# Kernel tuning notes

Measured on AMD Instinct MI355X. Metric: run time of the kernel, lower is better.

## Reference

```python
import jax, jax.numpy as jnp
import numpy as np

PAD_TOKEN = 0.0
REPLACEMENT_PROB = 0.1


def setup_inputs() -> dict:
    key = jax.random.key(0)
    # item-ID-like values in [0, 100000); zeros act as pad tokens
    x = jax.random.randint(key, (16384, 2048), 0, 100000).astype(jnp.float32)
    return {"x": x}


def reference(x):
    """Stochastic Swap Noise: replace ~p of non-pad positions with values
    sampled without replacement from the non-pad values of the tensor.

    Jit-friendly equivalent of torch's
      bernoulli -> masked_select compaction -> randperm -> scatter
    chain: a single argsort on random keys (pads keyed to +2.0) both
    compacts the non-pad values to the front AND shuffles them; a cumsum
    over the replacement mask assigns each replaced position its donor.
    """
    key = jax.random.key(42)
    k_bern, k_shuf = jax.random.split(key)

    nonpad = x != PAD_TOKEN                                        # [B,S] bool
    repl = (jax.random.uniform(k_bern, x.shape) < REPLACEMENT_PROB) & nonpad

    flat_x = x.reshape(-1)                                          # [N]
    flat_nonpad = nonpad.reshape(-1)
    flat_repl = repl.reshape(-1)

    # compaction + shuffle in one sort: non-pad elems get uniform [0,1) keys,
    # pads get 2.0 so they sink to the end.
    r = jnp.where(flat_nonpad, jax.random.uniform(k_shuf, flat_x.shape), 2.0)
    order = jnp.argsort(r)
    donors = flat_x[order]                                          # shuffled non-pad values first

    # k-th replaced position (in flat order) takes donors[k]
    rank = jnp.cumsum(flat_repl) - 1                                # -1 where not replaced (masked out below)
    out = jnp.where(flat_repl, donors[rank], flat_x)
    return out.reshape(x.shape)
```

## Files before the change

### kernel.cpp

```cpp
#include <hip/hip_runtime.h>
#include <stdint.h>

static __host__ __device__ inline uint32_t rotl32(uint32_t x, int r) {
#if defined(__HIP_DEVICE_COMPILE__)
  return __builtin_amdgcn_alignbit(x, x, (uint32_t)(32 - r));
#else
  return (x << r) | (x >> (32 - r));
#endif
}

static __host__ __device__ inline void tf2x32(uint32_t k0, uint32_t k1,
                                              uint32_t x0, uint32_t x1,
                                              uint32_t& o0, uint32_t& o1) {
  uint32_t k2 = k0 ^ k1 ^ 0x1BD11BDAu;
#define TFR(a) { x0 += x1; x1 = rotl32(x1, a); x1 ^= x0; }
  x0 += k0; x1 += k1;
  TFR(13) TFR(15) TFR(26) TFR(6)
  x0 += k1; x1 += k2 + 1u;
  TFR(17) TFR(29) TFR(16) TFR(24)
  x0 += k2; x1 += k0 + 2u;
  TFR(13) TFR(15) TFR(26) TFR(6)
  x0 += k0; x1 += k1 + 3u;
  TFR(17) TFR(29) TFR(16) TFR(24)
  x0 += k1; x1 += k2 + 4u;
  TFR(13) TFR(15) TFR(26) TFR(6)
  x0 += k2; x1 += k0 + 5u;
#undef TFR
  o0 = x0; o1 = x1;
}

static __device__ inline uint32_t fold_bits(uint32_t k0, uint32_t k1, uint32_t ctr) {
  uint32_t a, b;
  tf2x32(k0, k1, 0u, ctr, a, b);
  return a ^ b;
}

#define CUT2      917504u
#define NBINS2    896u
#define NH        1024
#define ELEMS_G   8192
#define GPOOL     1216u
#define BSCAP     4608u
#define WIN       8192
#define CAPDUMP   3932160u
#define STRIDE    4608u
#define MASKI     0x07FFFFFFu
#define BERN_THR  838861u



template<bool BOUNDS>
__global__ __launch_bounds__(256, 6) void k_gen(const float* __restrict__ x,
                                                uint64_t* __restrict__ mask,
                                                uint32_t* __restrict__ rsums,
                                                uint32_t* __restrict__ dumpCursor,
                                                uint2* __restrict__ dump,
                                                uint32_t bk0, uint32_t bk1,
                                                uint32_t sk0, uint32_t sk1, int n) {
  __shared__ uint2 pool[GPOOL];
  __shared__ uint32_t wcnt[4];
  __shared__ uint32_t lpoolCnt, lgbase;
  int tid = threadIdx.x, lane = tid & 63, wid = tid >> 6;
  int base = blockIdx.x * ELEMS_G;
  if (tid == 0) lpoolCnt = 0;
  __syncthreads();

  uint32_t cnt = 0;
  unsigned long long bball[4];
  for (int it = 0; it < ELEMS_G / 1024; it++) {
    int e0 = base + it * 1024 + wid * 256 + lane * 4;
    float4 xv;
    if (!BOUNDS || e0 + 3 < n) {
      xv = *reinterpret_cast<const float4*>(x + e0);
    } else {
      xv.x = (e0 + 0 < n) ? x[e0 + 0] : 0.0f;
      xv.y = (e0 + 1 < n) ? x[e0 + 1] : 0.0f;
      xv.z = (e0 + 2 < n) ? x[e0 + 2] : 0.0f;
      xv.w = (e0 + 3 < n) ? x[e0 + 3] : 0.0f;
    }
#define GENE(e, comp)                                                     \
    {                                                                     \
      uint32_t ii = (uint32_t)(e0 + e);                                   \
      bool np = (comp != 0.0f);                                           \
      uint32_t bb = fold_bits(bk0, bk1, ii);                              \
      bool rr = np && ((bb >> 9) < BERN_THR);                             \
      bball[e] = __ballot(rr);                                            \
      uint32_t mm = fold_bits(sk0, sk1, ii) >> 9;                         \
      if (np && mm < CUT2) {                                              \
        uint32_t slot = atomicAdd(&lpoolCnt, 1u);                         \
        uint32_t v = (uint32_t)comp;                                      \
        if (slot < GPOOL)                                                 \
          pool[slot] = make_uint2((mm << 12) | (v >> 5),                  \
                                  ((v & 31u) << 27) | ii);                \
      }                                                                   \
    }
    GENE(0, xv.x) GENE(1, xv.y) GENE(2, xv.z) GENE(3, xv.w)
#undef GENE
    cnt += (uint32_t)(__popcll(bball[0]) + __popcll(bball[1]) +
                      __popcll(bball[2]) + __popcll(bball[3]));
    if (lane == 0) {
      uint32_t ci = (uint32_t)blockIdx.x * 32u + (uint32_t)it * 4u + (uint32_t)wid;
      if (!BOUNDS) {
        mask[ci * 4 + 0] = bball[0]; mask[ci * 4 + 1] = bball[1];
        mask[ci * 4 + 2] = bball[2]; mask[ci * 4 + 3] = bball[3];
      } else {
        for (int e = 0; e < 4; e++)
          if ((int)(ci * 256u + (uint32_t)e * 64u) < n) mask[ci * 4 + e] = bball[e];
      }
    }
  }
  if (lane == 0) wcnt[wid] = cnt;
  __syncthreads();
  if (tid == 0) {
    rsums[blockIdx.x] = wcnt[0] + wcnt[1] + wcnt[2] + wcnt[3];
    uint32_t pc = lpoolCnt; if (pc > GPOOL) pc = GPOOL;
    lgbase = atomicAdd((unsigned int*)dumpCursor, pc);
  }
  __syncthreads();
  uint32_t pc = lpoolCnt; if (pc > GPOOL) pc = GPOOL;
  uint32_t gb = lgbase;
  for (uint32_t j = tid; j < pc; j += 256) {
    uint32_t d = gb + j;
    if (d < CAPDUMP) dump[d] = pool[j];
  }
}

__global__ void k_scan2(uint32_t* __restrict__ data0, int n0,
                        uint32_t* __restrict__ data1, int n1) {
  __shared__ uint32_t wsum[4];
  uint32_t* data = (blockIdx.x == 0) ? data0 : data1;
  int n = (blockIdx.x == 0) ? n0 : n1;
  int tid = threadIdx.x, lane = tid & 63, wid = tid >> 6;
  uint32_t running = 0;
  for (int base = 0; base < n; base += 256) {
    int i = base + tid;
    uint32_t v = (i < n) ? data[i] : 0u;
    uint32_t incl = v;
    for (int d = 1; d < 64; d <<= 1) {
      uint32_t t = __shfl_up(incl, (unsigned)d, 64);
      if (lane >= d) incl += t;
    }
    if (lane == 63) wsum[wid] = incl;
    __syncthreads();
    uint32_t woff = 0, tot = 0;
    for (int w = 0; w < 4; w++) { uint32_t s = wsum[w]; if (w < wid) woff += s; tot += s; }
    if (i < n) data[i] = running + woff + (incl - v);
    running += tot;
    __syncthreads();
  }
  if (tid == 0) data[n] = running;
}

__global__ __launch_bounds__(256) void k_regroup(const uint2* __restrict__ dump,
                                                 const uint32_t* __restrict__ dumpCursor,
                                                 uint32_t* __restrict__ fineCursor,
                                                 uint2* __restrict__ fine) {
  __shared__ uint2    pool2[WIN];
  __shared__ uint32_t lhist[NH];
  __shared__ uint32_t lgbase[NH];
  __shared__ uint32_t wsums[4];
  int tid = threadIdx.x, lane = tid & 63, wid = tid >> 6;
  uint32_t total = dumpCursor[0];
  if (total > CAPDUMP) total = CAPDUMP;
  uint32_t wbase = blockIdx.x * (uint32_t)WIN;
  if (wbase >= total) return;
  uint32_t valid = total - wbase;
  if (valid > WIN) valid = WIN;

  for (int b = tid; b < NH; b += 256) lhist[b] = 0;
  __syncthreads();
  uint2 e[WIN / 256];
#pragma unroll
  for (int q = 0; q < WIN / 256; q++) {
    uint32_t j = (uint32_t)q * 256u + (uint32_t)tid;
    e[q] = (j < valid) ? dump[wbase + j] : make_uint2(0u, 0u);
    if (j < valid) atomicAdd(&lhist[e[q].x >> 22], 1u);
  }
  __syncthreads();
  for (int b = tid; b < NH; b += 256) {
    uint32_t h = lhist[b];
    lgbase[b] = h ? atomicAdd((unsigned int*)&fineCursor[b], h) : 0u;
  }
  __syncthreads();
  uint32_t h0 = lhist[4 * tid], h1 = lhist[4 * tid + 1],
           h2 = lhist[4 * tid + 2], h3 = lhist[4 * tid + 3];
  uint32_t tsum = h0 + h1 + h2 + h3;
  uint32_t incl = tsum;
  for (int d = 1; d < 64; d <<= 1) {
    uint32_t t = __shfl_up(incl, (unsigned)d, 64);
    if (lane >= d) incl += t;
  }
  if (lane == 63) wsums[wid] = incl;
  __syncthreads();
  if (wid == 0) {
    uint32_t v = (lane < 4) ? wsums[lane] : 0u;
    uint32_t in2 = v;
    for (int d = 1; d < 4; d <<= 1) {
      uint32_t t = __shfl_up(in2, (unsigned)d, 64);
      if (lane >= d) in2 += t;
    }
    if (lane < 4) wsums[lane] = in2 - v;
  }
  __syncthreads();
  uint32_t texcl = wsums[wid] + (incl - tsum);
  uint32_t e0 = texcl, e1 = e0 + h0, e2 = e1 + h1, e3 = e2 + h2;
  __syncthreads();
  lhist[4 * tid] = e0; lhist[4 * tid + 1] = e1;
  lhist[4 * tid + 2] = e2; lhist[4 * tid + 3] = e3;
  __syncthreads();
#pragma unroll
  for (int q = 0; q < WIN / 256; q++) {
    uint32_t j = (uint32_t)q * 256u + (uint32_t)tid;
    if (j < valid) {
      uint32_t b = e[q].x >> 22;
      uint32_t lpos = atomicAdd(&lhist[b], 1u);
      pool2[lpos] = e[q];
    }
  }
  __syncthreads();
  for (uint32_t j = tid; j < valid; j += 256) {
    uint2 p = pool2[j];
    uint32_t b = p.x >> 22;
    uint32_t st = (b == 0) ? 0u : lhist[b - 1];
    uint32_t dst = lgbase[b] + (j - st);
    if (dst < STRIDE) fine[(size_t)b * STRIDE + dst] = p;
  }
}

__global__ __launch_bounds__(256) void k_binsort(const uint2* __restrict__ pairs,
                                                 const uint32_t* __restrict__ binPrefix,
                                                 float* __restrict__ donors) {
  __shared__ uint2    lbuf[BSCAP];
  __shared__ uint32_t hist[NH];
  __shared__ uint32_t wsums[4];
  int tid = threadIdx.x, lane = tid & 63, wid = tid >> 6;
  uint32_t bin = blockIdx.x;
  uint32_t gbase = binPrefix[bin];
  uint32_t cnt = binPrefix[bin + 1] - gbase;
  if (cnt > STRIDE) cnt = STRIDE;
  if (cnt > BSCAP) cnt = BSCAP;
  const uint2* src = pairs + (size_t)bin * STRIDE;

  for (int c = tid; c < 1024; c += 256) hist[c] = 0;
  __syncthreads();
  for (uint32_t j = tid; j < cnt; j += 256)
    atomicAdd(&hist[(src[j].x >> 12) & 1023u], 1u);
  __syncthreads();
  uint32_t h0 = hist[4 * tid], h1 = hist[4 * tid + 1],
           h2 = hist[4 * tid + 2], h3 = hist[4 * tid + 3];
  uint32_t tsum = h0 + h1 + h2 + h3;
  uint32_t incl = tsum;
  for (int d = 1; d < 64; d <<= 1) {
    uint32_t t = __shfl_up(incl, (unsigned)d, 64);
    if (lane >= d) incl += t;
  }
  if (lane == 63) wsums[wid] = incl;
  __syncthreads();
  if (wid == 0) {
    uint32_t v = (lane < 4) ? wsums[lane] : 0u;
    uint32_t in2 = v;
    for (int d = 1; d < 4; d <<= 1) {
      uint32_t t = __shfl_up(in2, (unsigned)d, 64);
      if (lane >= d) in2 += t;
    }
    if (lane < 4) wsums[lane] = in2 - v;
  }
  __syncthreads();
  uint32_t texcl = wsums[wid] + (incl - tsum);
  uint32_t e0 = texcl, e1 = e0 + h0, e2 = e1 + h1, e3 = e2 + h2;
  __syncthreads();
  hist[4 * tid] = e0; hist[4 * tid + 1] = e1;
  hist[4 * tid + 2] = e2; hist[4 * tid + 3] = e3;
  __syncthreads();
  for (uint32_t j = tid; j < cnt; j += 256) {
    uint2 p = src[j];
    uint32_t c = (p.x >> 12) & 1023u;
    uint32_t lpos = atomicAdd(&hist[c], 1u);
    lbuf[lpos] = p;
  }
  __syncthreads();
  for (int c = tid; c < 1024; c += 256) {
    uint32_t lo = (c == 0) ? 0u : hist[c - 1];
    uint32_t hi = hist[c];
    for (uint32_t u = lo + 1; u < hi; u++) {
      uint2 v = lbuf[u];
      uint32_t w = u;
      while (w > lo && (lbuf[w - 1].y & MASKI) > (v.y & MASKI)) {
        lbuf[w] = lbuf[w - 1];
        w--;
      }
      lbuf[w] = v;
    }
  }
  __syncthreads();
  for (uint32_t j = tid; j < cnt; j += 256) {
    uint2 p = lbuf[j];
    uint32_t v = ((p.x & 0xFFFu) << 5) | (p.y >> 27);
    donors[gbase + j] = (float)v;
  }
}

template<bool BOUNDS>
__global__ __launch_bounds__(256) void k_final(const float* __restrict__ x,
                                               const uint64_t* __restrict__ mask,
                                               const uint32_t* __restrict__ rsums,
                                               const float* __restrict__ donors,
                                               float* __restrict__ out, int n) {
  __shared__ uint64_t lw[ELEMS_G / 64];
  __shared__ uint32_t ctot[32], cpre[32];
  int tid = threadIdx.x, lane = tid & 63, wid = tid >> 6;
  int base = blockIdx.x * ELEMS_G;
  int wordBase = blockIdx.x * (ELEMS_G / 64);
  if (tid < ELEMS_G / 64) {
    uint64_t w = 0ull;
    int wI = wordBase + tid;
    if (!BOUNDS || (((wI >> 2) * 256) + ((wI & 3) * 64) < n)) w = mask[wI];
    lw[tid] = w;
  }
  __syncthreads();
  if (tid < 32) {
    ctot[tid] = (uint32_t)(__popcll(lw[4 * tid]) + __popcll(lw[4 * tid + 1]) +
                           __popcll(lw[4 * tid + 2]) + __popcll(lw[4 * tid + 3]));
  }
  __syncthreads();
  if (tid == 0) {
    uint32_t run = 0;
    for (int c = 0; c < 32; c++) { cpre[c] = run; run += ctot[c]; }
  }
  __syncthreads();
  uint32_t rbase = rsums[blockIdx.x];
  uint64_t lt = (1ull << lane) - 1ull;
  for (int it = 0; it < ELEMS_G / 1024; it++) {
    int c = it * 4 + wid;
    uint64_t b0 = lw[c * 4 + 0], b1 = lw[c * 4 + 1],
             b2 = lw[c * 4 + 2], b3 = lw[c * 4 + 3];
    uint32_t running = rbase + cpre[c];
    int e0 = base + it * 1024 + wid * 256 + lane * 4;
    uint32_t below = (uint32_t)(__popcll(b0 & lt) + __popcll(b1 & lt) +
                                __popcll(b2 & lt) + __popcll(b3 & lt));
    uint32_t r0 = (uint32_t)((b0 >> lane) & 1ull), r1 = (uint32_t)((b1 >> lane) & 1ull);
    uint32_t r2 = (uint32_t)((b2 >> lane) & 1ull), r3 = (uint32_t)((b3 >> lane) & 1ull);
    uint32_t rk = running + below;
    float4 xv;
    if (!BOUNDS || e0 + 3 < n) {
      xv = *reinterpret_cast<const float4*>(x + e0);
    } else {
      xv.x = (e0 + 0 < n) ? x[e0 + 0] : 0.0f;
      xv.y = (e0 + 1 < n) ? x[e0 + 1] : 0.0f;
      xv.z = (e0 + 2 < n) ? x[e0 + 2] : 0.0f;
      xv.w = (e0 + 3 < n) ? x[e0 + 3] : 0.0f;
    }
    float4 ov;
    ov.x = r0 ? donors[rk] : xv.x;               rk += r0;
    ov.y = r1 ? donors[rk] : xv.y;               rk += r1;
    ov.z = r2 ? donors[rk] : xv.z;               rk += r2;
    ov.w = r3 ? donors[rk] : xv.w;
    if (!BOUNDS || e0 + 3 < n) {
      *reinterpret_cast<float4*>(out + e0) = ov;
    } else {
      if (e0 + 0 < n) out[e0 + 0] = ov.x;
      if (e0 + 1 < n) out[e0 + 1] = ov.y;
      if (e0 + 2 < n) out[e0 + 2] = ov.z;
      if (e0 + 3 < n) out[e0 + 3] = ov.w;
    }
  }
}

extern "C" void kernel_launch(void* const* d_in, const int* in_sizes, int n_in,
                              void* d_out, int out_size, void* d_ws, size_t ws_size,
                              hipStream_t stream) {
  const float* x = (const float*)d_in[0];
  float* out = (float*)d_out;
  int n = in_sizes[0];
  (void)n_in; (void)out_size; (void)ws_size;

  uint32_t bk0, bk1, sk0, sk1;
  tf2x32(0u, 42u, 0u, 0u, bk0, bk1);
  tf2x32(0u, 42u, 0u, 1u, sk0, sk1);

  int nBlkG = (n + ELEMS_G - 1) / ELEMS_G;
  bool exact = ((n % ELEMS_G) == 0);

  size_t off = 0;
  auto alloc = [&](size_t bytes) -> void* {
    void* p = (uint8_t*)d_ws + off;
    off += (bytes + 255) & ~(size_t)255;
    return p;
  };
  uint32_t* dumpCursor = (uint32_t*)alloc(4);
  uint32_t* fineCursor = (uint32_t*)alloc((size_t)(NH + 1) * 4);
  uint32_t* rsums      = (uint32_t*)alloc((size_t)(nBlkG + 1) * 4);
  uint64_t* mask       = (uint64_t*)alloc((size_t)((n + 63) / 64 + 4) * 8);
  uint2*    dump       = (uint2*)alloc((size_t)CAPDUMP * 8);
  uint2*    fine       = (uint2*)alloc((size_t)NBINS2 * STRIDE * 8);
  float*    donors     = (float*)dump;

  hipMemsetAsync(dumpCursor, 0, (size_t)(NH + 2) * 4 + 512, stream);

  if (exact)
    k_gen<false><<<nBlkG, 256, 0, stream>>>(x, mask, rsums, dumpCursor, dump,
                                            bk0, bk1, sk0, sk1, n);
  else
    k_gen<true><<<nBlkG, 256, 0, stream>>>(x, mask, rsums, dumpCursor, dump,
                                           bk0, bk1, sk0, sk1, n);
  int nWin = (int)((CAPDUMP + WIN - 1) / WIN);
  k_regroup<<<nWin, 256, 0, stream>>>(dump, dumpCursor, fineCursor, fine);
  k_scan2<<<2, 256, 0, stream>>>(rsums, nBlkG, fineCursor, (int)NBINS2);
  k_binsort<<<(int)NBINS2, 256, 0, stream>>>(fine, fineCursor, donors);
  if (exact)
    k_final<false><<<nBlkG, 256, 0, stream>>>(x, mask, rsums, donors, out, n);
  else
    k_final<true><<<nBlkG, 256, 0, stream>>>(x, mask, rsums, donors, out, n);
}
```

Baseline: 338.4 us.

## Double coarse sort bins, halve windows, and aggregate pool atomics per wavefront

Raises the number of coarse regroup bins from 896 to 1792 by taking one more key bit, and halves the per-bin capacity and the regroup window size. The per-bin sort kernel now uses a 512-entry fine histogram and sorts smaller buckets in LDS, so more blocks run with less shared memory each. In k_gen, each lane's own shared atomic for pool slots is replaced by a wavefront ballot with one atomic per wave and a popcount offset per lane. The memset now zeroes exactly the cursor region. Smaller bins with the same tail margin raise the risk of overflowing STRIDE.

```diff
diff --git a/kernel.cpp b/kernel.cpp
--- a/kernel.cpp
+++ b/kernel.cpp
@@ -36,27 +36,27 @@
 }
 
 #define CUT2      917504u
-#define NBINS2    896u
-#define NH        1024
+#define NBINS2    1792u
+#define NH        2048
 #define ELEMS_G   8192
 #define GPOOL     1216u
-#define BSCAP     4608u
-#define WIN       8192
+#define BSCAP     2432u
+#define WIN       4096
 #define CAPDUMP   3932160u
-#define STRIDE    4608u
+#define STRIDE    2432u
 #define MASKI     0x07FFFFFFu
 #define BERN_THR  838861u
 
 
 
 template<bool BOUNDS>
-__global__ __launch_bounds__(256, 6) void k_gen(const float* __restrict__ x,
-                                                uint64_t* __restrict__ mask,
-                                                uint32_t* __restrict__ rsums,
-                                                uint32_t* __restrict__ dumpCursor,
-                                                uint2* __restrict__ dump,
-                                                uint32_t bk0, uint32_t bk1,
-                                                uint32_t sk0, uint32_t sk1, int n) {
+__global__ __launch_bounds__(256) void k_gen(const float* __restrict__ x,
+                                             uint64_t* __restrict__ mask,
+                                             uint32_t* __restrict__ rsums,
+                                             uint32_t* __restrict__ dumpCursor,
+                                             uint2* __restrict__ dump,
+                                             uint32_t bk0, uint32_t bk1,
+                                             uint32_t sk0, uint32_t sk1, int n) {
   __shared__ uint2 pool[GPOOL];
   __shared__ uint32_t wcnt[4];
   __shared__ uint32_t lpoolCnt, lgbase;
@@ -66,6 +66,7 @@
   __syncthreads();
 
   uint32_t cnt = 0;
+  uint64_t lt = (1ull << lane) - 1ull;
   unsigned long long bball[4];
   for (int it = 0; it < ELEMS_G / 1024; it++) {
     int e0 = base + it * 1024 + wid * 256 + lane * 4;
@@ -86,12 +87,18 @@
       bool rr = np && ((bb >> 9) < BERN_THR);                             \
       bball[e] = __ballot(rr);                                            \
       uint32_t mm = fold_bits(sk0, sk1, ii) >> 9;                         \
-      if (np && mm < CUT2) {                                              \
-        uint32_t slot = atomicAdd(&lpoolCnt, 1u);                         \
-        uint32_t v = (uint32_t)comp;                                      \
-        if (slot < GPOOL)                                                 \
+      bool cand = np && (mm < CUT2);                                      \
+      unsigned long long cb = __ballot(cand);                             \
+      uint32_t pb = 0;                                                    \
+      if (lane == 0 && cb) pb = atomicAdd(&lpoolCnt, (uint32_t)__popcll(cb)); \
+      pb = __builtin_amdgcn_readfirstlane(pb);                            \
+      if (cand) {                                                         \
+        uint32_t slot = pb + (uint32_t)__popcll(cb & lt);                 \
+        if (slot < GPOOL) {                                               \
+          uint32_t v = (uint32_t)comp;                                    \
           pool[slot] = make_uint2((mm << 12) | (v >> 5),                  \
                                   ((v & 31u) << 27) | ii);                \
+        }                                                                 \
       }                                                                   \
     }
     GENE(0, xv.x) GENE(1, xv.y) GENE(2, xv.z) GENE(3, xv.w)
@@ -174,7 +181,7 @@
   for (int q = 0; q < WIN / 256; q++) {
     uint32_t j = (uint32_t)q * 256u + (uint32_t)tid;
     e[q] = (j < valid) ? dump[wbase + j] : make_uint2(0u, 0u);
-    if (j < valid) atomicAdd(&lhist[e[q].x >> 22], 1u);
+    if (j < valid) atomicAdd(&lhist[e[q].x >> 21], 1u);
   }
   __syncthreads();
   for (int b = tid; b < NH; b += 256) {
@@ -182,9 +189,9 @@
     lgbase[b] = h ? atomicAdd((unsigned int*)&fineCursor[b], h) : 0u;
   }
   __syncthreads();
-  uint32_t h0 = lhist[4 * tid], h1 = lhist[4 * tid + 1],
-           h2 = lhist[4 * tid + 2], h3 = lhist[4 * tid + 3];
-  uint32_t tsum = h0 + h1 + h2 + h3;
+  uint32_t hv[8], tsum = 0;
+#pragma unroll
+  for (int j = 0; j < 8; j++) { hv[j] = lhist[8 * tid + j]; tsum += hv[j]; }
   uint32_t incl = tsum;
   for (int d = 1; d < 64; d <<= 1) {
     uint32_t t = __shfl_up(incl, (unsigned)d, 64);
@@ -202,17 +209,15 @@
     if (lane < 4) wsums[lane] = in2 - v;
   }
   __syncthreads();
-  uint32_t texcl = wsums[wid] + (incl - tsum);
-  uint32_t e0 = texcl, e1 = e0 + h0, e2 = e1 + h1, e3 = e2 + h2;
-  __syncthreads();
-  lhist[4 * tid] = e0; lhist[4 * tid + 1] = e1;
-  lhist[4 * tid + 2] = e2; lhist[4 * tid + 3] = e3;
+  uint32_t run = wsums[wid] + (incl - tsum);
+#pragma unroll
+  for (int j = 0; j < 8; j++) { uint32_t h = hv[j]; lhist[8 * tid + j] = run; run += h; }
   __syncthreads();
 #pragma unroll
   for (int q = 0; q < WIN / 256; q++) {
     uint32_t j = (uint32_t)q * 256u + (uint32_t)tid;
     if (j < valid) {
-      uint32_t b = e[q].x >> 22;
+      uint32_t b = e[q].x >> 21;
       uint32_t lpos = atomicAdd(&lhist[b], 1u);
       pool2[lpos] = e[q];
     }
@@ -220,7 +225,7 @@
   __syncthreads();
   for (uint32_t j = tid; j < valid; j += 256) {
     uint2 p = pool2[j];
-    uint32_t b = p.x >> 22;
+    uint32_t b = p.x >> 21;
     uint32_t st = (b == 0) ? 0u : lhist[b - 1];
     uint32_t dst = lgbase[b] + (j - st);
     if (dst < STRIDE) fine[(size_t)b * STRIDE + dst] = p;
@@ -231,7 +236,7 @@
                                                  const uint32_t* __restrict__ binPrefix,
                                                  float* __restrict__ donors) {
   __shared__ uint2    lbuf[BSCAP];
-  __shared__ uint32_t hist[NH];
+  __shared__ uint32_t hist[512];
   __shared__ uint32_t wsums[4];
   int tid = threadIdx.x, lane = tid & 63, wid = tid >> 6;
   uint32_t bin = blockIdx.x;
@@ -241,14 +246,13 @@
   if (cnt > BSCAP) cnt = BSCAP;
   const uint2* src = pairs + (size_t)bin * STRIDE;
 
-  for (int c = tid; c < 1024; c += 256) hist[c] = 0;
+  for (int c = tid; c < 512; c += 256) hist[c] = 0;
   __syncthreads();
   for (uint32_t j = tid; j < cnt; j += 256)
-    atomicAdd(&hist[(src[j].x >> 12) & 1023u], 1u);
-  __syncthreads();
-  uint32_t h0 = hist[4 * tid], h1 = hist[4 * tid + 1],
-           h2 = hist[4 * tid + 2], h3 = hist[4 * tid + 3];
-  uint32_t tsum = h0 + h1 + h2 + h3;
+    atomicAdd(&hist[(src[j].x >> 12) & 511u], 1u);
+  __syncthreads();
+  uint32_t h0 = hist[2 * tid], h1 = hist[2 * tid + 1];
+  uint32_t tsum = h0 + h1;
   uint32_t incl = tsum;
   for (int d = 1; d < 64; d <<= 1) {
     uint32_t t = __shfl_up(incl, (unsigned)d, 64);
@@ -267,19 +271,18 @@
   }
   __syncthreads();
   uint32_t texcl = wsums[wid] + (incl - tsum);
-  uint32_t e0 = texcl, e1 = e0 + h0, e2 = e1 + h1, e3 = e2 + h2;
-  __syncthreads();
-  hist[4 * tid] = e0; hist[4 * tid + 1] = e1;
-  hist[4 * tid + 2] = e2; hist[4 * tid + 3] = e3;
+  uint32_t e0 = texcl, e1 = e0 + h0;
+  __syncthreads();
+  hist[2 * tid] = e0; hist[2 * tid + 1] = e1;
   __syncthreads();
   for (uint32_t j = tid; j < cnt; j += 256) {
     uint2 p = src[j];
-    uint32_t c = (p.x >> 12) & 1023u;
+    uint32_t c = (p.x >> 12) & 511u;
     uint32_t lpos = atomicAdd(&hist[c], 1u);
     lbuf[lpos] = p;
   }
   __syncthreads();
-  for (int c = tid; c < 1024; c += 256) {
+  for (int c = tid; c < 512; c += 256) {
     uint32_t lo = (c == 0) ? 0u : hist[c - 1];
     uint32_t hi = hist[c];
     for (uint32_t u = lo + 1; u < hi; u++) {
@@ -389,13 +392,14 @@
   };
   uint32_t* dumpCursor = (uint32_t*)alloc(4);
   uint32_t* fineCursor = (uint32_t*)alloc((size_t)(NH + 1) * 4);
+  size_t zeroBytes = off;
   uint32_t* rsums      = (uint32_t*)alloc((size_t)(nBlkG + 1) * 4);
   uint64_t* mask       = (uint64_t*)alloc((size_t)((n + 63) / 64 + 4) * 8);
   uint2*    dump       = (uint2*)alloc((size_t)CAPDUMP * 8);
   uint2*    fine       = (uint2*)alloc((size_t)NBINS2 * STRIDE * 8);
   float*    donors     = (float*)dump;
 
-  hipMemsetAsync(dumpCursor, 0, (size_t)(NH + 2) * 4 + 512, stream);
+  hipMemsetAsync(d_ws, 0, zeroBytes, stream);
 
   if (exact)
     k_gen<false><<<nBlkG, 256, 0, stream>>>(x, mask, rsums, dumpCursor, dump,
```

Measured after the change: 334.9 us. About the same (-1.0%).
